# Optimization experiments

Hardware: AMD Instinct MI355X
Metric: run time of the kernel (lower is better)

Reference implementation:

```python
import jax, jax.numpy as jnp
import numpy as np
from jax import lax

C = 256
POOL = 7
NUM_CLASSES = 81
D = NUM_CLASSES - 1
STRIDES = (4, 8, 16, 32)
DEC_MULT = (0.1, 0.1, 0.2, 0.2)  # decode_settings: multipliers on raw deltas
LOG_MAX = float(np.log(1000.0 / 16.0))


def setup_inputs() -> dict:
    key = jax.random.key(0)
    ks = jax.random.split(key, 16)
    n, Rp = 2, 512
    R = n * Rp
    img = 800.0
    cx = jax.random.uniform(ks[0], (R,), minval=0.0, maxval=img)
    cy = jax.random.uniform(ks[1], (R,), minval=0.0, maxval=img)
    w = jax.random.uniform(ks[2], (R,), minval=16.0, maxval=300.0)
    h = jax.random.uniform(ks[3], (R,), minval=16.0, maxval=300.0)
    x1 = jnp.clip(cx - w / 2, 0.0, img - 1.0)
    y1 = jnp.clip(cy - h / 2, 0.0, img - 1.0)
    x2 = jnp.minimum(jnp.maximum(cx + w / 2, x1 + 1.0), img)
    y2 = jnp.minimum(jnp.maximum(cy + h / 2, y1 + 1.0), img)
    proposals = jnp.stack([x1, y1, x2, y2], -1)
    imidx = jnp.repeat(jnp.arange(n, dtype=jnp.int32), Rp)
    fmaps = {}
    for li, s in enumerate(STRIDES):
        hw = int(800 // s)
        fmaps[f"fmap{li}"] = jax.random.normal(ks[4 + li], (n, hw, hw, C), jnp.float32)
    c1, clin = C * POOL * POOL, 1024
    def lin(k, fi, fo):
        return (jax.random.normal(k, (fi, fo), jnp.float32) / np.sqrt(fi).astype(np.float32),
                jnp.zeros((fo,), jnp.float32))
    W0, b0 = lin(ks[8], c1, clin)
    W1, b1 = lin(ks[9], clin, clin)
    Wc, bc = lin(ks[10], clin, NUM_CLASSES)
    Wr, br = lin(ks[11], clin, NUM_CLASSES * 4)
    imsizes = jnp.full((n, 2), img, jnp.float32)  # (h, w) per image
    return dict(proposals=proposals, imidx=imidx, **fmaps,
                W0=W0, b0=b0, W1=W1, b1=b1, Wc=Wc, bc=bc, Wr=Wr, br=br,
                imsizes=imsizes, score_thr=0.05, iou_thr=0.5, imtop=100, min_size=1.0)


def _roi_align_level(fmap, boxes, imidx, stride):
    # fmap [n,H,W,C], boxes [R,4] xyxy in image coords; 1 sample per bin, bilinear.
    n, H, W, c = fmap.shape
    s = 1.0 / stride
    x1, y1, x2, y2 = boxes[:, 0] * s, boxes[:, 1] * s, boxes[:, 2] * s, boxes[:, 3] * s
    g = (jnp.arange(POOL, dtype=jnp.float32) + 0.5) / POOL  # bin centers in [0,1]
    xs = x1[:, None] + g[None, :] * (x2 - x1)[:, None] - 0.5  # [R,POOL]
    ys = y1[:, None] + g[None, :] * (y2 - y1)[:, None] - 0.5
    R = boxes.shape[0]
    xx = jnp.broadcast_to(xs[:, None, :], (R, POOL, POOL))
    yy = jnp.broadcast_to(ys[:, :, None], (R, POOL, POOL))
    x0f, y0f = jnp.floor(xx), jnp.floor(yy)
    wx, wy = xx - x0f, yy - y0f
    x0 = jnp.clip(x0f.astype(jnp.int32), 0, W - 1)
    x1i = jnp.clip(x0f.astype(jnp.int32) + 1, 0, W - 1)
    y0 = jnp.clip(y0f.astype(jnp.int32), 0, H - 1)
    y1i = jnp.clip(y0f.astype(jnp.int32) + 1, 0, H - 1)
    ii = imidx[:, None, None]
    v00 = fmap[ii, y0, x0]; v01 = fmap[ii, y0, x1i]
    v10 = fmap[ii, y1i, x0]; v11 = fmap[ii, y1i, x1i]  # each [R,POOL,POOL,C]
    wx, wy = wx[..., None], wy[..., None]
    return (v00 * (1 - wx) * (1 - wy) + v01 * wx * (1 - wy)
            + v10 * (1 - wx) * wy + v11 * wx * wy)


def _forward(proposals, imidx, fmaps, W0, b0, W1, b1, Wc, bc, Wr, br,
             imsizes, score_thr, iou_thr, imtop, min_size):
    R = proposals.shape[0]
    pw = proposals[:, 2] - proposals[:, 0]
    ph = proposals[:, 3] - proposals[:, 1]
    # FPN level assignment (torchvision canonical formula)
    lvl = jnp.floor(4.0 + jnp.log2(jnp.sqrt(pw * ph) / 224.0 + 1e-6))
    lvl = jnp.clip(lvl, 2, 5).astype(jnp.int32) - 2
    pooled = jnp.zeros((R, POOL, POOL, C), fmaps[0].dtype)
    for k, (fm, st) in enumerate(zip(fmaps, STRIDES)):
        pk = _roi_align_level(fm, proposals, imidx, st)
        pooled = jnp.where((lvl == k)[:, None, None, None], pk, pooled)
    # two-FC head + cls/reg
    x = pooled.reshape(R, -1)
    x = jax.nn.relu(x @ W0 + b0)
    x = jax.nn.relu(x @ W1 + b1)
    reg = (x @ Wr + br).reshape(R, NUM_CLASSES, 4)[:, 1:]      # [R,D,4]
    scr = jax.nn.softmax(x @ Wc + bc, axis=-1)[:, 1:]          # [R,D]
    cls = jnp.broadcast_to(jnp.arange(1, NUM_CLASSES, dtype=jnp.int32), (R, D))
    # decode boxes (proposal cwh + weighted deltas, log-space clamp)
    cx = (proposals[:, 0] + proposals[:, 2]) * 0.5
    cy = (proposals[:, 1] + proposals[:, 3]) * 0.5
    dx = reg[..., 0] * DEC_MULT[0]
    dy = reg[..., 1] * DEC_MULT[1]
    dw = jnp.minimum(reg[..., 2] * DEC_MULT[2], LOG_MAX)
    dh = jnp.minimum(reg[..., 3] * DEC_MULT[3], LOG_MAX)
    ncx = dx * pw[:, None] + cx[:, None]
    ncy = dy * ph[:, None] + cy[:, None]
    nw = jnp.exp(dw) * pw[:, None]
    nh = jnp.exp(dh) * ph[:, None]
    hb = imsizes[imidx, 0][:, None]
    wb = imsizes[imidx, 1][:, None]
    bx1 = jnp.clip(ncx - nw / 2, 0.0, wb); bx2 = jnp.clip(ncx + nw / 2, 0.0, wb)
    by1 = jnp.clip(ncy - nh / 2, 0.0, hb); by2 = jnp.clip(ncy + nh / 2, 0.0, hb)
    boxes = jnp.stack([bx1, by1, bx2, by2], -1)                # [R,D,4]
    valid = (scr > score_thr) & (bx2 - bx1 >= min_size) & (by2 - by1 >= min_size)
    # flatten roi-class pairs; class-offset boxes = torchvision batched_nms trick
    M = R * D
    boxes_f = boxes.reshape(M, 4)
    scr_f = scr.reshape(M)
    cls_f = cls.reshape(M)
    valid_f = valid.reshape(M)
    imidx_f = jnp.repeat(imidx, D)
    off = cls_f.astype(boxes_f.dtype)[:, None] * (jnp.max(imsizes) + 2.0)
    bo = boxes_f + off
    areas = (bo[:, 2] - bo[:, 0]) * (bo[:, 3] - bo[:, 1])
    def nms(scores0):
        def step(scores, _):
            i = jnp.argmax(scores)
            s = scores[i]
            b = bo[i]
            iw = jnp.clip(jnp.minimum(b[2], bo[:, 2]) - jnp.maximum(b[0], bo[:, 0]), 0.0)
            ih = jnp.clip(jnp.minimum(b[3], bo[:, 3]) - jnp.maximum(b[1], bo[:, 1]), 0.0)
            inter = iw * ih
            iou = inter / (areas[i] + areas - inter + 1e-6)
            scores = jnp.where(iou > iou_thr, -1.0, scores)
            scores = scores.at[i].set(-1.0)
            return scores, (i, s)
        _, (idx, s) = lax.scan(step, scores0, None, length=imtop)
        return idx, s
    n = imsizes.shape[0]
    ob, osc, ocl = [], [], []
    for i in range(n):
        s0 = jnp.where(valid_f & (imidx_f == i), scr_f, -1.0)
        idx, s = nms(s0)
        keep = s > 0.0  # padded slots have score <= 0
        ob.append(jnp.where(keep[:, None], boxes_f[idx], 0.0))
        osc.append(jnp.where(keep, s, 0.0))
        ocl.append(jnp.where(keep, cls_f[idx], -1))
    return jnp.stack(ob), jnp.stack(osc), jnp.stack(ocl)


def reference(proposals, imidx, fmap0, fmap1, fmap2, fmap3, W0, b0, W1, b1,
              Wc, bc, Wr, br, imsizes, score_thr, iou_thr, imtop, min_size):
    return _forward(proposals, imidx, (fmap0, fmap1, fmap2, fmap3), W0, b0, W1,
                    b1, Wc, bc, Wr, br, imsizes, score_thr, iou_thr, int(imtop),
                    min_size)
```

## Files before the change

kernel.cpp:

```cpp
#include <hip/hip_runtime.h>
#include <math.h>

#define CCH 256
#define NPOOL 7
#define NCLS 81
#define DCLS 80
#define NHEAD 512
#define FLOG_MAX 4.1351666f

typedef _Float16 half8 __attribute__((ext_vector_type(8)));
typedef _Float16 half4 __attribute__((ext_vector_type(4)));
typedef float floatx4 __attribute__((ext_vector_type(4)));

__global__ void zero_k(float4* __restrict__ p, int count4)
{
    int i = blockIdx.x * blockDim.x + threadIdx.x;
    if (i < count4) p[i] = make_float4(0.f, 0.f, 0.f, 0.f);
}

__device__ __forceinline__ void roi_setup(
    const float* __restrict__ prop, const int* __restrict__ imidx,
    const float* __restrict__ f0, const float* __restrict__ f1,
    const float* __restrict__ f2, const float* __restrict__ f3,
    int h0, int h1, int h2, int h3, int b,
    const float*& base, int& W, size_t& o00, size_t& o01, size_t& o10, size_t& o11,
    float& w00, float& w01, float& w10, float& w11)
{
    int roi = b / 49, p = b % 49;
    int py = p / 7, px = p % 7;

    const float* pr = prop + (size_t)roi * 4;
    float x1 = pr[0], y1 = pr[1], x2 = pr[2], y2 = pr[3];
    float pw = x2 - x1, ph = y2 - y1;

    float lv = floorf(4.0f + log2f(sqrtf(pw * ph) / 224.0f + 1e-6f));
    lv = fminf(fmaxf(lv, 2.0f), 5.0f);
    int lvl = (int)lv - 2;

    const float* fm; int H; float s;
    if (lvl == 0)      { fm = f0; H = h0; s = 0.25f;    }
    else if (lvl == 1) { fm = f1; H = h1; s = 0.125f;   }
    else if (lvl == 2) { fm = f2; H = h2; s = 0.0625f;  }
    else               { fm = f3; H = h3; s = 0.03125f; }
    W = H;

    float xs1 = x1 * s, ys1 = y1 * s, xs2 = x2 * s, ys2 = y2 * s;
    float gx = (px + 0.5f) / 7.0f, gy = (py + 0.5f) / 7.0f;
    float xx = xs1 + gx * (xs2 - xs1) - 0.5f;
    float yy = ys1 + gy * (ys2 - ys1) - 0.5f;
    float x0f = floorf(xx), y0f = floorf(yy);
    float wx = xx - x0f, wy = yy - y0f;
    int x0i = min(max((int)x0f, 0), W - 1);
    int x1i = min(max((int)x0f + 1, 0), W - 1);
    int y0i = min(max((int)y0f, 0), H - 1);
    int y1i = min(max((int)y0f + 1, 0), H - 1);

    int ii = imidx[roi];
    base = fm + (size_t)ii * H * W * CCH;
    o00 = ((size_t)y0i * W + x0i) * CCH;
    o01 = ((size_t)y0i * W + x1i) * CCH;
    o10 = ((size_t)y1i * W + x0i) * CCH;
    o11 = ((size_t)y1i * W + x1i) * CCH;
    w00 = (1.0f - wx) * (1.0f - wy);
    w01 = wx * (1.0f - wy);
    w10 = (1.0f - wx) * wy;
    w11 = wx * wy;
}

__global__ void roi_align_k(const float* __restrict__ prop,
                            const int* __restrict__ imidx,
                            const float* __restrict__ f0,
                            const float* __restrict__ f1,
                            const float* __restrict__ f2,
                            const float* __restrict__ f3,
                            int h0, int h1, int h2, int h3,
                            float* __restrict__ pooled)
{
    int b = blockIdx.x, c = threadIdx.x;
    const float* base; int W; size_t o00, o01, o10, o11;
    float w00, w01, w10, w11;
    roi_setup(prop, imidx, f0, f1, f2, f3, h0, h1, h2, h3, b,
              base, W, o00, o01, o10, o11, w00, w01, w10, w11);
    float v = base[o00 + c] * w00 + base[o01 + c] * w01
            + base[o10 + c] * w10 + base[o11 + c] * w11;
    pooled[(size_t)b * CCH + c] = v;
}

__device__ __forceinline__ void roi_f16v4_body(
    const float* __restrict__ prop, const int* __restrict__ imidx,
    const float* __restrict__ f0, const float* __restrict__ f1,
    const float* __restrict__ f2, const float* __restrict__ f3,
    int h0, int h1, int h2, int h3, int bb, int t,
    _Float16* __restrict__ poolH, _Float16* __restrict__ poolL)
{
    int b = bb * 4 + (t >> 6);
    int lane = t & 63;
    const float* base; int W; size_t o00, o01, o10, o11;
    float w00, w01, w10, w11;
    roi_setup(prop, imidx, f0, f1, f2, f3, h0, h1, h2, h3, b,
              base, W, o00, o01, o10, o11, w00, w01, w10, w11);

    int c4 = lane * 4;
    float4 v00 = *(const float4*)(base + o00 + c4);
    float4 v01 = *(const float4*)(base + o01 + c4);
    float4 v10 = *(const float4*)(base + o10 + c4);
    float4 v11 = *(const float4*)(base + o11 + c4);
    const float* p00 = (const float*)&v00;
    const float* p01 = (const float*)&v01;
    const float* p10 = (const float*)&v10;
    const float* p11 = (const float*)&v11;

    half4 h, l;
#pragma unroll
    for (int e = 0; e < 4; ++e) {
        float v = p00[e] * w00 + p01[e] * w01 + p10[e] * w10 + p11[e] * w11;
        _Float16 hh = (_Float16)v;
        h[e] = hh;
        l[e] = (_Float16)(v - (float)hh);
    }
    size_t idx = (size_t)b * CCH + c4;
    *(half4*)(poolH + idx) = h;
    *(half4*)(poolL + idx) = l;
}

__device__ __forceinline__ void conv_fast_body(
    const float* __restrict__ W, _Float16* __restrict__ WtH,
    _Float16* __restrict__ WtL, int K, int N, int k0, int n0, int t,
    float (*sh)[65])
{
#pragma unroll
    for (int p = 0; p < 4; ++p) {
        int idx = p * 256 + t;
        int kr = idx >> 4, nc = (idx & 15) * 4;
        float4 v = *(const float4*)(W + (size_t)(k0 + kr) * N + n0 + nc);
        sh[kr][nc + 0] = v.x; sh[kr][nc + 1] = v.y;
        sh[kr][nc + 2] = v.z; sh[kr][nc + 3] = v.w;
    }
    __syncthreads();
#pragma unroll
    for (int p = 0; p < 4; ++p) {
        int idx = p * 256 + t;
        int nr = idx >> 4, kc = (idx & 15) * 4;
        half4 h, l;
#pragma unroll
        for (int i = 0; i < 4; ++i) {
            float v = sh[kc + i][nr];
            _Float16 hh = (_Float16)v;
            h[i] = hh;
            l[i] = (_Float16)(v - (float)hh);
        }
        *(half4*)(WtH + (size_t)(n0 + nr) * K + k0 + kc) = h;
        *(half4*)(WtL + (size_t)(n0 + nr) * K + k0 + kc) = l;
    }
}

__device__ __forceinline__ void conv_guard_body(
    const float* __restrict__ W, _Float16* __restrict__ WtH,
    _Float16* __restrict__ WtL, int K, int N, int Kt, int rowofs,
    int k0, int n0, int t, float (*sh)[65])
{
#pragma unroll
    for (int p = 0; p < 4; ++p) {
        int idx = p * 256 + t;
        int kr = idx >> 4, nc = (idx & 15) * 4;
#pragma unroll
        for (int e = 0; e < 4; ++e) {
            int nn = n0 + nc + e;
            sh[kr][nc + e] = (nn < N) ? W[(size_t)(k0 + kr) * N + nn] : 0.0f;
        }
    }
    __syncthreads();
#pragma unroll
    for (int p = 0; p < 4; ++p) {
        int idx = p * 256 + t;
        int nr = idx >> 4, kc = (idx & 15) * 4;
        if (n0 + nr < N) {
            half4 h, l;
#pragma unroll
            for (int i = 0; i < 4; ++i) {
                float v = sh[kc + i][nr];
                _Float16 hh = (_Float16)v;
                h[i] = hh;
                l[i] = (_Float16)(v - (float)hh);
            }
            *(half4*)(WtH + (size_t)(rowofs + n0 + nr) * Kt + k0 + kc) = h;
            *(half4*)(WtL + (size_t)(rowofs + n0 + nr) * Kt + k0 + kc) = l;
        }
    }
}

__global__ __launch_bounds__(256) void pre_uber_k(
    const float* __restrict__ prop, const int* __restrict__ imidx,
    const float* __restrict__ f0, const float* __restrict__ f1,
    const float* __restrict__ f2, const float* __restrict__ f3,
    int h0, int h1, int h2, int h3,
    _Float16* __restrict__ poolH, _Float16* __restrict__ poolL,
    const float* __restrict__ W0, _Float16* __restrict__ W0tH, _Float16* __restrict__ W0tL,
    const float* __restrict__ W1, _Float16* __restrict__ W1tH, _Float16* __restrict__ W1tL,
    const float* __restrict__ Wc, const float* __restrict__ Wr,
    _Float16* __restrict__ WheadtH, _Float16* __restrict__ WheadtL,
    float4* __restrict__ zp, int zc4,
    int* __restrict__ cntp, int ncnt,
    int R, int K0, int CL)
{
    __shared__ float sh[64][65];
    int b = blockIdx.x, t = threadIdx.x;

    if (blockIdx.x == 0 && t < ncnt) cntp[t] = 0;

    int NB_ROI = (R * 49) / 4;
    int KT0 = K0 / 64, NT0 = CL / 64;
    int NB_CW0 = KT0 * NT0;
    int KT1 = CL / 64;
    int NB_CW1 = KT1 * KT1;
    int NTc = (NCLS + 63) / 64;
    int NB_CWc = KT1 * NTc;
    int NTr = (NCLS * 4 + 63) / 64;
    int NB_CWr = KT1 * NTr;

    if (b < NB_ROI) {
        roi_f16v4_body(prop, imidx, f0, f1, f2, f3, h0, h1, h2, h3, b, t,
                       poolH, poolL);
        return;
    }
    b -= NB_ROI;
    if (b < NB_CW0) {
        int k0 = (b % KT0) * 64, n0 = (b / KT0) * 64;
        conv_fast_body(W0, W0tH, W0tL, K0, CL, k0, n0, t, sh);
        return;
    }
    b -= NB_CW0;
    if (b < NB_CW1) {
        int k0 = (b % KT1) * 64, n0 = (b / KT1) * 64;
        conv_fast_body(W1, W1tH, W1tL, CL, CL, k0, n0, t, sh);
        return;
    }
    b -= NB_CW1;
    if (b < NB_CWc) {
        int k0 = (b % KT1) * 64, n0 = (b / KT1) * 64;
        conv_guard_body(Wc, WheadtH, WheadtL, CL, NCLS, CL, 0, k0, n0, t, sh);
        return;
    }
    b -= NB_CWc;
    if (b < NB_CWr) {
        int k0 = (b % KT1) * 64, n0 = (b / KT1) * 64;
        conv_guard_body(Wr, WheadtH, WheadtL, CL, NCLS * 4, CL, NCLS, k0, n0, t, sh);
        return;
    }
    b -= NB_CWr;
    {
        int i = b * 256 + t;
        if (i < zc4) zp[i] = make_float4(0.f, 0.f, 0.f, 0.f);
    }
}

__global__ void act_split_k(const float* __restrict__ acc,
                            const float* __restrict__ bias,
                            _Float16* __restrict__ outH,
                            _Float16* __restrict__ outL,
                            int total, int CL)
{
    int i = (blockIdx.x * blockDim.x + threadIdx.x) * 4;
    if (i >= total) return;
    int b = i % CL;
    float4 v = *(const float4*)(acc + i);
    float4 bb = *(const float4*)(bias + b);
    const float* pv = (const float*)&v;
    const float* pb = (const float*)&bb;
    half4 h, l;
#pragma unroll
    for (int e = 0; e < 4; ++e) {
        float f = fmaxf(pv[e] + pb[e], 0.0f);
        _Float16 hh = (_Float16)f;
        h[e] = hh;
        l[e] = (_Float16)(f - (float)hh);
    }
    *(half4*)(outH + i) = h;
    *(half4*)(outL + i) = l;
}

__device__ __forceinline__ void dma16(const _Float16* g, _Float16* l)
{
    __builtin_amdgcn_global_load_lds(
        (const __attribute__((address_space(1))) unsigned int*)g,
        (__attribute__((address_space(3))) unsigned int*)l, 16, 0, 0);
}

#define LDKE 32
#define DKQ_SWZ(lane)  ((((lane) & 3) ^ (((lane) >> 3) & 3)) << 3)
#define FK_SWZ(lane)   (((((lane) >> 4) ^ (((lane) >> 1) & 3))) << 3)

__global__ __launch_bounds__(256) void gemm_mfma_split_k(
    const _Float16* __restrict__ Ah, const _Float16* __restrict__ Al,
    const _Float16* __restrict__ Bh, const _Float16* __restrict__ Bl,
    float* __restrict__ Cacc, int M, int N, int K, int Kc, int SP)
{
    __shared__ _Float16 sAh[128 * LDKE], sAl[128 * LDKE];
    __shared__ _Float16 sBh[64 * LDKE],  sBl[64 * LDKE];

    int bid = blockIdx.x;
    int z = bid % SP;
    int q = bid / SP;
    int NT = N >> 6;
    int nn = q % NT;
    int m = q / NT;
    int m0 = m * 128, n0 = nn * 64;
    int kb = z * Kc;
    int ke = min(K, kb + Kc);

    int t = threadIdx.x;
    int lane = t & 63, w = t >> 6;
    int wr = w >> 1, wc = w & 1;
    int fr = lane & 15;
    int fk = FK_SWZ(lane);

    int drowA = w * 32 + (lane >> 2);
    int drowB = w * 16 + (lane >> 2);
    int dkq = DKQ_SWZ(lane);
    const _Float16* gAh = Ah + (size_t)(m0 + drowA) * K + dkq;
    const _Float16* gAl = Al + (size_t)(m0 + drowA) * K + dkq;
    const _Float16* gBh = Bh + (size_t)(n0 + drowB) * K + dkq;
    const _Float16* gBl = Bl + (size_t)(n0 + drowB) * K + dkq;
    size_t rowskip = (size_t)16 * K;

    _Float16* lAh0 = &sAh[(w * 2 + 0) * 512];
    _Float16* lAh1 = &sAh[(w * 2 + 1) * 512];
    _Float16* lAl0 = &sAl[(w * 2 + 0) * 512];
    _Float16* lAl1 = &sAl[(w * 2 + 1) * 512];
    _Float16* lBh  = &sBh[w * 512];
    _Float16* lBl  = &sBl[w * 512];

    floatx4 acc[4][2] = {};

    for (int k0 = kb; k0 < ke; k0 += 32) {
        dma16(gAh + k0, lAh0);
        dma16(gAh + rowskip + k0, lAh1);
        dma16(gAl + k0, lAl0);
        dma16(gAl + rowskip + k0, lAl1);
        dma16(gBh + k0, lBh);
        dma16(gBl + k0, lBl);
        __syncthreads();

        half8 ah[4], al[4], bh[2], bl[2];
#pragma unroll
        for (int i = 0; i < 4; ++i) {
            int ar = wr * 64 + i * 16 + fr;
            ah[i] = *(const half8*)&sAh[ar * LDKE + fk];
            al[i] = *(const half8*)&sAl[ar * LDKE + fk];
        }
#pragma unroll
        for (int j = 0; j < 2; ++j) {
            int bcc = wc * 32 + j * 16 + fr;
            bh[j] = *(const half8*)&sBh[bcc * LDKE + fk];
            bl[j] = *(const half8*)&sBl[bcc * LDKE + fk];
        }
#pragma unroll
        for (int i = 0; i < 4; ++i)
#pragma unroll
            for (int j = 0; j < 2; ++j) {
                acc[i][j] = __builtin_amdgcn_mfma_f32_16x16x32_f16(ah[i], bh[j], acc[i][j], 0, 0, 0);
                acc[i][j] = __builtin_amdgcn_mfma_f32_16x16x32_f16(ah[i], bl[j], acc[i][j], 0, 0, 0);
                acc[i][j] = __builtin_amdgcn_mfma_f32_16x16x32_f16(al[i], bh[j], acc[i][j], 0, 0, 0);
            }
        __syncthreads();
    }

    int rbase = (lane >> 4) * 4;
#pragma unroll
    for (int i = 0; i < 4; ++i)
#pragma unroll
        for (int j = 0; j < 2; ++j) {
            int col = n0 + wc * 32 + j * 16 + fr;
#pragma unroll
            for (int r = 0; r < 4; ++r) {
                int row = m0 + wr * 64 + i * 16 + rbase + r;
                atomicAdd(&Cacc[(size_t)row * N + col], acc[i][j][r]);
            }
        }
}

__global__ __launch_bounds__(256) void gemm_mfma_fused64_k(
    const _Float16* __restrict__ Ah, const _Float16* __restrict__ Al,
    const _Float16* __restrict__ Bh, const _Float16* __restrict__ Bl,
    const float* __restrict__ bias,
    float* __restrict__ Cout,
    _Float16* __restrict__ outH, _Float16* __restrict__ outL,
    int M, int N, int K, int mode)
{
    __shared__ _Float16 sAh[2][64 * LDKE], sAl[2][64 * LDKE];
    __shared__ _Float16 sBh[2][64 * LDKE], sBl[2][64 * LDKE];

    int m0 = blockIdx.y * 64, n0 = blockIdx.x * 64;
    int t = threadIdx.x;
    int lane = t & 63, w = t >> 6;
    int wr = w >> 1, wc = w & 1;
    int fr = lane & 15;
    int fk = FK_SWZ(lane);

    int drow = w * 16 + (lane >> 2);
    int dkq = DKQ_SWZ(lane);
    const _Float16* gAh = Ah + (size_t)(m0 + drow) * K + dkq;
    const _Float16* gAl = Al + (size_t)(m0 + drow) * K + dkq;
    const _Float16* gBh = Bh + (size_t)(n0 + drow) * K + dkq;
    const _Float16* gBl = Bl + (size_t)(n0 + drow) * K + dkq;
    int lofs = w * 512;

    int nt = K >> 5;

    dma16(gAh + 0, &sAh[0][lofs]);
    dma16(gAl + 0, &sAl[0][lofs]);
    dma16(gBh + 0, &sBh[0][lofs]);
    dma16(gBl + 0, &sBl[0][lofs]);
    __syncthreads();

    floatx4 acc[2][2] = {};

    for (int tt = 0; tt < nt; ++tt) {
        int c = tt & 1, nb = c ^ 1;
        if (tt + 1 < nt) {
            int k1 = (tt + 1) << 5;
            dma16(gAh + k1, &sAh[nb][lofs]);
            dma16(gAl + k1, &sAl[nb][lofs]);
            dma16(gBh + k1, &sBh[nb][lofs]);
            dma16(gBl + k1, &sBl[nb][lofs]);
        }

        half8 ah[2], av[2], bh[2], bv[2];
#pragma unroll
        for (int i = 0; i < 2; ++i) {
            int ar = wr * 32 + i * 16 + fr;
            ah[i] = *(const half8*)&sAh[c][ar * LDKE + fk];
            av[i] = *(const half8*)&sAl[c][ar * LDKE + fk];
            int bc = wc * 32 + i * 16 + fr;
            bh[i] = *(const half8*)&sBh[c][bc * LDKE + fk];
            bv[i] = *(const half8*)&sBl[c][bc * LDKE + fk];
        }
#pragma unroll
        for (int i = 0; i < 2; ++i)
#pragma unroll
            for (int j = 0; j < 2; ++j) {
                acc[i][j] = __builtin_amdgcn_mfma_f32_16x16x32_f16(ah[i], bh[j], acc[i][j], 0, 0, 0);
                acc[i][j] = __builtin_amdgcn_mfma_f32_16x16x32_f16(ah[i], bv[j], acc[i][j], 0, 0, 0);
                acc[i][j] = __builtin_amdgcn_mfma_f32_16x16x32_f16(av[i], bh[j], acc[i][j], 0, 0, 0);
            }
        __syncthreads();
    }

    int rbase = (lane >> 4) * 4;
#pragma unroll
    for (int i = 0; i < 2; ++i)
#pragma unroll
        for (int j = 0; j < 2; ++j) {
            int col = n0 + wc * 32 + j * 16 + fr;
#pragma unroll
            for (int r = 0; r < 4; ++r) {
                int row = m0 + wr * 32 + i * 16 + rbase + r;
                float v = acc[i][j][r];
                if (mode == 0) {
                    Cout[(size_t)row * N + col] = v;
                } else {
                    float f = fmaxf(v + bias[col], 0.0f);
                    _Float16 hh = (_Float16)f;
                    outH[(size_t)row * N + col] = hh;
                    outL[(size_t)row * N + col] = (_Float16)(f - (float)hh);
                }
            }
        }
}

__global__ __launch_bounds__(256) void gemm_splitk_k(const float* __restrict__ A,
                                                     const float* __restrict__ B,
                                                     const float* __restrict__ abias,
                                                     float* __restrict__ Cacc,
                                                     int M, int N, int K, int Kc)
{
    __shared__ float Ast[16][68];
    __shared__ float Bs[16][68];

    int m0 = blockIdx.y * 64, n0 = blockIdx.x * 64;
    int kb = blockIdx.z * Kc;
    int ke = min(K, kb + Kc);
    int tid = threadIdx.x;
    int tx = tid & 15, ty = tid >> 4;
    int arow = tid >> 2, akq = (tid & 3) << 2;
    int bcol = tid & 63, bk = tid >> 6;

    const float* Arow = A + (size_t)(m0 + arow) * K;
    bool nfull = (n0 + 64 <= N);

    float acc[4][4] = {};

    for (int k0 = kb; k0 < ke; k0 += 16) {
        float4 av = *(const float4*)(Arow + k0 + akq);
        if (abias) {
            av.x = fmaxf(av.x + abias[k0 + akq + 0], 0.0f);
            av.y = fmaxf(av.y + abias[k0 + akq + 1], 0.0f);
            av.z = fmaxf(av.z + abias[k0 + akq + 2], 0.0f);
            av.w = fmaxf(av.w + abias[k0 + akq + 3], 0.0f);
        }
        float bv[4];
        if (nfull) {
#pragma unroll
            for (int e = 0; e < 4; ++e)
                bv[e] = B[(size_t)(k0 + bk * 4 + e) * N + n0 + bcol];
        } else {
            bool ok = (n0 + bcol) < N;
#pragma unroll
            for (int e = 0; e < 4; ++e)
                bv[e] = ok ? B[(size_t)(k0 + bk * 4 + e) * N + n0 + bcol] : 0.0f;
        }
        __syncthreads();
        Ast[akq + 0][arow] = av.x;
        Ast[akq + 1][arow] = av.y;
        Ast[akq + 2][arow] = av.z;
        Ast[akq + 3][arow] = av.w;
#pragma unroll
        for (int e = 0; e < 4; ++e) Bs[bk * 4 + e][bcol] = bv[e];
        __syncthreads();

#pragma unroll
        for (int kk = 0; kk < 16; ++kk) {
            float4 af = *(const float4*)&Ast[kk][ty * 4];
            float4 bf = *(const float4*)&Bs[kk][tx * 4];
            float a_[4] = {af.x, af.y, af.z, af.w};
            float b_[4] = {bf.x, bf.y, bf.z, bf.w};
#pragma unroll
            for (int i = 0; i < 4; ++i)
#pragma unroll
                for (int j = 0; j < 4; ++j)
                    acc[i][j] = fmaf(a_[i], b_[j], acc[i][j]);
        }
    }

#pragma unroll
    for (int i = 0; i < 4; ++i) {
        int row = m0 + ty * 4 + i;
#pragma unroll
        for (int j = 0; j < 4; ++j) {
            int col = n0 + tx * 4 + j;
            if (col < N) atomicAdd(&Cacc[(size_t)row * N + col], acc[i][j]);
        }
    }
}

__global__ void softmax_k(const float* __restrict__ logits, int ldl,
                          const float* __restrict__ bc,
                          float* __restrict__ scr)
{
    int r = blockIdx.x;
    int t = threadIdx.x;
    const float* row = logits + (size_t)r * ldl;

    float v0 = row[t] + bc[t];
    float v1 = (t + 64 < NCLS) ? (row[t + 64] + bc[t + 64]) : -INFINITY;
    float m = fmaxf(v0, v1);
#pragma unroll
    for (int o = 32; o > 0; o >>= 1) m = fmaxf(m, __shfl_down(m, o));
    m = __shfl(m, 0);

    float e0 = expf(v0 - m);
    float e1 = (t + 64 < NCLS) ? expf(v1 - m) : 0.0f;
    float sum = e0 + e1;
#pragma unroll
    for (int o = 32; o > 0; o >>= 1) sum += __shfl_down(sum, o);
    sum = __shfl(sum, 0);
    float inv = 1.0f / sum;

    if (t >= 1)        scr[(size_t)r * DCLS + (t - 1)]  = e0 * inv;
    if (t + 64 < NCLS) scr[(size_t)r * DCLS + (t + 63)] = e1 * inv;
}

__global__ __launch_bounds__(256) void compact_k(
    const float* __restrict__ head, int ldh, int regofs,
    const float* __restrict__ bc,
    const float* __restrict__ br,
    const float* __restrict__ prop,
    const int* __restrict__ imidx,
    const float* __restrict__ imsz,
    const float* __restrict__ score_thr_p,
    const float* __restrict__ min_size_p,
    int* __restrict__ cntp,
    int* __restrict__ cidx,
    float* __restrict__ cscore,
    float* __restrict__ cbo,
    float* __restrict__ cbox,
    float* __restrict__ carea,
    int M, int n, int R)
{
    int wid = threadIdx.x >> 6, t = threadIdx.x & 63;
    int r = blockIdx.x * 4 + wid;
    if (r >= R) return;

    const float* row = head + (size_t)r * ldh;
    float v0 = row[t] + bc[t];
    float v1 = (t + 64 < NCLS) ? (row[t + 64] + bc[t + 64]) : -INFINITY;
    float m = fmaxf(v0, v1);
#pragma unroll
    for (int o = 32; o > 0; o >>= 1) m = fmaxf(m, __shfl_down(m, o));
    m = __shfl(m, 0);

    float e0 = expf(v0 - m);
    float e1 = (t + 64 < NCLS) ? expf(v1 - m) : 0.0f;
    float sum = e0 + e1;
#pragma unroll
    for (int o = 32; o > 0; o >>= 1) sum += __shfl_down(sum, o);
    sum = __shfl(sum, 0);
    float inv = 1.0f / sum;

    float score_thr = score_thr_p[0];
    float min_size  = min_size_p[0];
    float immax = imsz[0];
    for (int q = 1; q < 2 * n; ++q) immax = fmaxf(immax, imsz[q]);

    int img = imidx[r];
    int base = img * M;
    const float* pr = prop + (size_t)r * 4;
    float pw = pr[2] - pr[0], ph = pr[3] - pr[1];
    float cx = (pr[0] + pr[2]) * 0.5f, cy = (pr[1] + pr[3]) * 0.5f;
    float hbound = imsz[img * 2 + 0];
    float wbound = imsz[img * 2 + 1];

#pragma unroll
    for (int pass = 0; pass < 2; ++pass) {
        int cls; float s; bool active;
        if (pass == 0) { cls = t;      s = e0 * inv; active = (t >= 1); }
        else           { cls = t + 64; s = e1 * inv; active = (t + 64 < NCLS); }
        if (!active || s <= score_thr) continue;

        const float* rg_ = head + (size_t)r * ldh + regofs + cls * 4;
        const float* bb = br + cls * 4;
        float dx = (rg_[0] + bb[0]) * 0.1f;
        float dy = (rg_[1] + bb[1]) * 0.1f;
        float dw = fminf((rg_[2] + bb[2]) * 0.2f, FLOG_MAX);
        float dh = fminf((rg_[3] + bb[3]) * 0.2f, FLOG_MAX);
        float ncx = dx * pw + cx;
        float ncy = dy * ph + cy;
        float nw = expf(dw) * pw;
        float nh = expf(dh) * ph;
        float bx1 = fminf(fmaxf(ncx - nw * 0.5f, 0.0f), wbound);
        float bx2 = fminf(fmaxf(ncx + nw * 0.5f, 0.0f), wbound);
        float by1 = fminf(fmaxf(ncy - nh * 0.5f, 0.0f), hbound);
        float by2 = fminf(fmaxf(ncy + nh * 0.5f, 0.0f), hbound);
        if (bx2 - bx1 < min_size || by2 - by1 < min_size) continue;

        float off = (float)cls * (immax + 2.0f);
        int j = r * DCLS + cls - 1;
        int p = atomicAdd(&cntp[img], 1);
        cidx[base + p] = j;
        cscore[base + p] = s;
        cbox[(size_t)(base + p) * 4 + 0] = bx1;
        cbox[(size_t)(base + p) * 4 + 1] = by1;
        cbox[(size_t)(base + p) * 4 + 2] = bx2;
        cbox[(size_t)(base + p) * 4 + 3] = by2;
        cbo[(size_t)(base + p) * 4 + 0] = bx1 + off;
        cbo[(size_t)(base + p) * 4 + 1] = by1 + off;
        cbo[(size_t)(base + p) * 4 + 2] = bx2 + off;
        cbo[(size_t)(base + p) * 4 + 3] = by2 + off;
        carea[base + p] = (bx2 - bx1) * (by2 - by1);
    }
}

#define NMS_T 1024
#define NMS_SORTMAX 4096
#define NMS_AMAX 512
__global__ __launch_bounds__(NMS_T) void nms_pick_k(
    const float* __restrict__ iou_thr_p,
    const int* __restrict__ cntp,
    int* __restrict__ cidx,
    float* __restrict__ cscore,
    float* __restrict__ cbo,
    float* __restrict__ cbox,
    float* __restrict__ carea,
    float* __restrict__ out,
    int M, int n, int imtop)
{
// ... 144 lines not shown
                    if (os > b2 || (os == b2 && og < g2)) { b2 = os; g2 = og; l2 = ol; }
                }
                if (lane == 0) {
                    f_sc = b2;
                    if (b2 > 0.0f) {
                        int lp = l2;
                        size_t oslot = (size_t)img * imtop + it;
                        ob[oslot * 4 + 0] = cbox[(size_t)(base + lp) * 4 + 0];
                        ob[oslot * 4 + 1] = cbox[(size_t)(base + lp) * 4 + 1];
                        ob[oslot * 4 + 2] = cbox[(size_t)(base + lp) * 4 + 2];
                        ob[oslot * 4 + 3] = cbox[(size_t)(base + lp) * 4 + 3];
                        osc[oslot] = b2;
                        ocl[oslot] = (float)(g2 % DCLS + 1);
                        f_o0 = cbo[(size_t)(base + lp) * 4 + 0];
                        f_o1 = cbo[(size_t)(base + lp) * 4 + 1];
                        f_o2 = cbo[(size_t)(base + lp) * 4 + 2];
                        f_o3 = cbo[(size_t)(base + lp) * 4 + 3];
                        f_ar = carea[base + lp];
                        cscore[base + lp] = -1.0f;
                    }
                }
            }
            __syncthreads();
            if (f_sc <= 0.0f) break;

            float b0 = f_o0, b1 = f_o1, b2_ = f_o2, b3 = f_o3, ai = f_ar;
            for (int p = t; p < K; p += T) {
                float c0 = cbo[(size_t)(base + p) * 4 + 0];
                float c1 = cbo[(size_t)(base + p) * 4 + 1];
                float c2 = cbo[(size_t)(base + p) * 4 + 2];
                float c3 = cbo[(size_t)(base + p) * 4 + 3];
                float iw = fmaxf(fminf(b2_, c2) - fmaxf(b0, c0), 0.0f);
                float ih = fmaxf(fminf(b3, c3) - fmaxf(b1, c1), 0.0f);
                float inter = iw * ih;
                float iou = inter / (ai + carea[base + p] - inter + 1e-6f);
                if (iou > iou_thr) cscore[base + p] = -1.0f;
            }
            __syncthreads();
        }
    }

    for (int q = it + t; q < imtop; q += T) {
        size_t oslot = (size_t)img * imtop + q;
        ob[oslot * 4 + 0] = 0.0f;
        ob[oslot * 4 + 1] = 0.0f;
        ob[oslot * 4 + 2] = 0.0f;
        ob[oslot * 4 + 3] = 0.0f;
        osc[oslot] = 0.0f;
        ocl[oslot] = -1.0f;
    }
}

__global__ __launch_bounds__(NMS_T) void nms_k(
    const float* __restrict__ scr,
    const float* __restrict__ prop,
    const int* __restrict__ imidx,
    const float* __restrict__ head, int ldh, int regofs,
    const float* __restrict__ br,
    const float* __restrict__ imsz,
    const float* __restrict__ score_thr_p,
    const float* __restrict__ min_size_p,
    const float* __restrict__ iou_thr_p,
    int* __restrict__ cidx,
    float* __restrict__ cscore,
    float* __restrict__ cbo,
    float* __restrict__ cbox,
    float* __restrict__ carea,
    float* __restrict__ out,
    int M, int n, int imtop)
{
    int img = blockIdx.x;
    int t = threadIdx.x;
    const int T = NMS_T;
    const int NW = NMS_T / 64;
    int lane = t & 63, wid = t >> 6;

    __shared__ int cnt;
    __shared__ float ws_sc[NW];
    __shared__ int ws_g[NW], ws_p[NW];
    __shared__ float f_sc, f_o0, f_o1, f_o2, f_o3, f_ar;

    if (t == 0) cnt = 0;
    __syncthreads();

    float score_thr = score_thr_p[0];
    float min_size  = min_size_p[0];
    float iou_thr   = iou_thr_p[0];
    float immax = imsz[0];
    for (int q = 1; q < 2 * n; ++q) immax = fmaxf(immax, imsz[q]);

    int base = img * M;
    for (int j = t; j < M; j += T) {
        int r = j / DCLS;
        if (imidx[r] != img) continue;
        float s = scr[j];
        if (s <= score_thr) continue;

        int cls = j - r * DCLS + 1;
        const float* pr = prop + (size_t)r * 4;
        float pw = pr[2] - pr[0], ph = pr[3] - pr[1];
        float cx = (pr[0] + pr[2]) * 0.5f, cy = (pr[1] + pr[3]) * 0.5f;
        const float* rg_ = head + (size_t)r * ldh + regofs + cls * 4;
        const float* bb = br + cls * 4;
        float dx = (rg_[0] + bb[0]) * 0.1f;
        float dy = (rg_[1] + bb[1]) * 0.1f;
        float dw = fminf((rg_[2] + bb[2]) * 0.2f, FLOG_MAX);
        float dh = fminf((rg_[3] + bb[3]) * 0.2f, FLOG_MAX);
        float ncx = dx * pw + cx;
        float ncy = dy * ph + cy;
        float nw = expf(dw) * pw;
        float nh = expf(dh) * ph;
        float hbound = imsz[img * 2 + 0];
        float wbound = imsz[img * 2 + 1];
        float bx1 = fminf(fmaxf(ncx - nw * 0.5f, 0.0f), wbound);
        float bx2 = fminf(fmaxf(ncx + nw * 0.5f, 0.0f), wbound);
        float by1 = fminf(fmaxf(ncy - nh * 0.5f, 0.0f), hbound);
        float by2 = fminf(fmaxf(ncy + nh * 0.5f, 0.0f), hbound);
        if (bx2 - bx1 < min_size || by2 - by1 < min_size) continue;

        float off = (float)cls * (immax + 2.0f);
        int p = atomicAdd(&cnt, 1);
        cidx[base + p] = j;
        cscore[base + p] = s;
        cbox[(size_t)(base + p) * 4 + 0] = bx1;
        cbox[(size_t)(base + p) * 4 + 1] = by1;
        cbox[(size_t)(base + p) * 4 + 2] = bx2;
        cbox[(size_t)(base + p) * 4 + 3] = by2;
        cbo[(size_t)(base + p) * 4 + 0] = bx1 + off;
        cbo[(size_t)(base + p) * 4 + 1] = by1 + off;
        cbo[(size_t)(base + p) * 4 + 2] = bx2 + off;
        cbo[(size_t)(base + p) * 4 + 3] = by2 + off;
        carea[base + p] = (bx2 - bx1) * (by2 - by1);
    }
    __syncthreads();
    int K = cnt;

    float* ob  = out;
    float* osc = out + (size_t)n * imtop * 4;
    float* ocl = out + (size_t)n * imtop * 5;

    int it = 0;
    for (; it < imtop; ++it) {
        float best = -1e30f; int bg = 0x7fffffff; int bl = -1;
        for (int p = t; p < K; p += T) {
            float sv = cscore[base + p];
            int g = cidx[base + p];
            if (sv > best || (sv == best && g < bg)) { best = sv; bg = g; bl = p; }
        }
#pragma unroll
        for (int o = 32; o > 0; o >>= 1) {
            float os = __shfl_down(best, o);
            int   og = __shfl_down(bg, o);
            int   ol = __shfl_down(bl, o);
            if (os > best || (os == best && og < bg)) { best = os; bg = og; bl = ol; }
        }
        if (lane == 0) { ws_sc[wid] = best; ws_g[wid] = bg; ws_p[wid] = bl; }
        __syncthreads();
        if (wid == 0) {
            float b2 = (lane < NW) ? ws_sc[lane] : -1e30f;
            int   g2 = (lane < NW) ? ws_g[lane] : 0x7fffffff;
            int   l2 = (lane < NW) ? ws_p[lane] : -1;
#pragma unroll
            for (int o = NW / 2; o > 0; o >>= 1) {
                float os = __shfl_down(b2, o);
                int   og = __shfl_down(g2, o);
                int   ol = __shfl_down(l2, o);
                if (os > b2 || (os == b2 && og < g2)) { b2 = os; g2 = og; l2 = ol; }
            }
            if (lane == 0) {
                f_sc = b2;
                if (b2 > 0.0f) {
                    int lp = l2;
                    size_t oslot = (size_t)img * imtop + it;
                    ob[oslot * 4 + 0] = cbox[(size_t)(base + lp) * 4 + 0];
                    ob[oslot * 4 + 1] = cbox[(size_t)(base + lp) * 4 + 1];
                    ob[oslot * 4 + 2] = cbox[(size_t)(base + lp) * 4 + 2];
                    ob[oslot * 4 + 3] = cbox[(size_t)(base + lp) * 4 + 3];
                    osc[oslot] = b2;
                    ocl[oslot] = (float)(g2 % DCLS + 1);
                    f_o0 = cbo[(size_t)(base + lp) * 4 + 0];
                    f_o1 = cbo[(size_t)(base + lp) * 4 + 1];
                    f_o2 = cbo[(size_t)(base + lp) * 4 + 2];
                    f_o3 = cbo[(size_t)(base + lp) * 4 + 3];
                    f_ar = carea[base + lp];
                    cscore[base + lp] = -1.0f;
                }
            }
        }
        __syncthreads();
        if (f_sc <= 0.0f) break;

        float b0 = f_o0, b1 = f_o1, b2_ = f_o2, b3 = f_o3, ai = f_ar;
        for (int p = t; p < K; p += T) {
            float c0 = cbo[(size_t)(base + p) * 4 + 0];
            float c1 = cbo[(size_t)(base + p) * 4 + 1];
            float c2 = cbo[(size_t)(base + p) * 4 + 2];
            float c3 = cbo[(size_t)(base + p) * 4 + 3];
            float iw = fmaxf(fminf(b2_, c2) - fmaxf(b0, c0), 0.0f);
            float ih = fmaxf(fminf(b3, c3) - fmaxf(b1, c1), 0.0f);
            float inter = iw * ih;
            float iou = inter / (ai + carea[base + p] - inter + 1e-6f);
            if (iou > iou_thr) cscore[base + p] = -1.0f;
        }
        __syncthreads();
    }

    for (int q = it + t; q < imtop; q += T) {
        size_t oslot = (size_t)img * imtop + q;
        ob[oslot * 4 + 0] = 0.0f;
        ob[oslot * 4 + 1] = 0.0f;
        ob[oslot * 4 + 2] = 0.0f;
        ob[oslot * 4 + 3] = 0.0f;
        osc[oslot] = 0.0f;
        ocl[oslot] = -1.0f;
    }
}

extern "C" void kernel_launch(void* const* d_in, const int* in_sizes, int n_in,
                              void* d_out, int out_size, void* d_ws, size_t ws_size,
                              hipStream_t stream)
{
    const float* prop   = (const float*)d_in[0];
    const int*   imidx  = (const int*)d_in[1];
    const float* f0     = (const float*)d_in[2];
    const float* f1     = (const float*)d_in[3];
    const float* f2     = (const float*)d_in[4];
    const float* f3     = (const float*)d_in[5];
    const float* W0     = (const float*)d_in[6];
    const float* b0     = (const float*)d_in[7];
    const float* W1     = (const float*)d_in[8];
    const float* b1     = (const float*)d_in[9];
    const float* Wc     = (const float*)d_in[10];
    const float* bc     = (const float*)d_in[11];
    const float* Wr     = (const float*)d_in[12];
    const float* br     = (const float*)d_in[13];
    const float* imsz   = (const float*)d_in[14];
    const float* sthr   = (const float*)d_in[15];
    const float* ithr   = (const float*)d_in[16];
    const float* msz    = (const float*)d_in[18];

    int R = in_sizes[1];
    int n = in_sizes[14] / 2;
    int imtop = out_size / (n * 6);
    int M = R * DCLS;
    int K0 = NPOOL * NPOOL * CCH;
    int CL = in_sizes[7];

    int h0 = (int)(sqrtf((float)(in_sizes[2] / (n * CCH))) + 0.5f);
    int h1 = (int)(sqrtf((float)(in_sizes[3] / (n * CCH))) + 0.5f);
    int h2 = (int)(sqrtf((float)(in_sizes[4] / (n * CCH))) + 0.5f);
    int h3 = (int)(sqrtf((float)(in_sizes[5] / (n * CCH))) + 0.5f);

    float* outf = (float*)d_out;

    size_t szPool  = (size_t)R * K0 * 2;
    size_t szX     = (size_t)R * CL * 4;
    size_t szHead  = (size_t)R * NHEAD * 4;
    size_t szWh    = (size_t)NHEAD * CL * 2;
    size_t szXh    = (size_t)R * CL * 2;
    size_t szW1t   = (size_t)CL * CL * 2;
    size_t szScr   = (size_t)R * DCLS * 4;

    size_t needed = 4 * szPool + 2 * szX + szHead + 2 * szWh
                  + 4 * szXh + 2 * szW1t + szScr;

    int splitK0 = 8;
    bool mfma_ok = (ws_size >= needed) && (R % 128 == 0) && (CL % 128 == 0)
                 && (K0 % (splitK0 * 32) == 0) && (CL % 32 == 0)
                 && ((R * 49) % 4 == 0) && (K0 % 64 == 0) && (CL % 64 == 0)
                 && (R % 4 == 0);

    if (mfma_ok) {
        uint8_t* w = (uint8_t*)d_ws;
        size_t o = 0;
        _Float16* poolH   = (_Float16*)(w + o); o += szPool;
        _Float16* poolL   = (_Float16*)(w + o); o += szPool;
        _Float16* W0tH    = (_Float16*)(w + o); o += szPool;
        _Float16* W0tL    = (_Float16*)(w + o); o += szPool;
        float*    x0acc   = (float*)(w + o);    o += szX;
        float*    unused  = (float*)(w + o);    o += szX;
        float*    headacc = (float*)(w + o);    o += szHead;
        _Float16* WheadtH = (_Float16*)(w + o); o += szWh;
        _Float16* WheadtL = (_Float16*)(w + o); o += szWh;
        _Float16* x0H     = (_Float16*)(w + o); o += szXh;
        _Float16* x0L     = (_Float16*)(w + o); o += szXh;
        _Float16* x1H     = (_Float16*)(w + o); o += szXh;
        _Float16* x1L     = (_Float16*)(w + o); o += szXh;
        _Float16* W1tH    = (_Float16*)(w + o); o += szW1t;
        _Float16* W1tL    = (_Float16*)(w + o); o += szW1t;
        float*    scr     = (float*)(w + o);
        (void)unused;

        int* cnt = (int*)scr;

        int*   cidx   = (int*)d_ws;
        float* cscore = (float*)(cidx + (size_t)n * M);
        float* cbo    = cscore + (size_t)n * M;
        float* cbox   = cbo + (size_t)n * M * 4;
        float* carea  = cbox + (size_t)n * M * 4;

        {
            int NB_ROI = (R * 49) / 4;
            int NB_CW0 = (K0 / 64) * (CL / 64);
            int NB_CW1 = (CL / 64) * (CL / 64);
            int NB_CWc = (CL / 64) * ((NCLS + 63) / 64);
            int NB_CWr = (CL / 64) * ((NCLS * 4 + 63) / 64);
            int zc4    = (int)(szX / 16);
            int NB_Z   = (zc4 + 255) / 256;
            int NB = NB_ROI + NB_CW0 + NB_CW1 + NB_CWc + NB_CWr + NB_Z;
            pre_uber_k<<<dim3(NB), dim3(256), 0, stream>>>(
                prop, imidx, f0, f1, f2, f3, h0, h1, h2, h3,
                poolH, poolL,
                W0, W0tH, W0tL,
                W1, W1tH, W1tL,
                Wc, Wr, WheadtH, WheadtL,
                (float4*)x0acc, zc4,
                cnt, n,
                R, K0, CL);
        }
        gemm_mfma_split_k<<<dim3(splitK0 * (R / 128) * (CL / 64)), dim3(256), 0, stream>>>(
            poolH, poolL, W0tH, W0tL, x0acc, R, CL, K0, K0 / splitK0, splitK0);
        act_split_k<<<dim3((R * CL / 4 + 255) / 256), dim3(256), 0, stream>>>(
            x0acc, b0, x0H, x0L, R * CL, CL);
        gemm_mfma_fused64_k<<<dim3(CL / 64, R / 64), dim3(256), 0, stream>>>(
            x0H, x0L, W1tH, W1tL, b1, nullptr, x1H, x1L, R, CL, CL, 1);
        gemm_mfma_fused64_k<<<dim3(NHEAD / 64, R / 64), dim3(256), 0, stream>>>(
            x1H, x1L, WheadtH, WheadtL, nullptr, headacc, nullptr, nullptr, R, NHEAD, CL, 0);
        compact_k<<<dim3(R / 4), dim3(256), 0, stream>>>(
            headacc, NHEAD, NCLS, bc, br, prop, imidx, imsz, sthr, msz,
            cnt, cidx, cscore, cbo, cbox, carea, M, n, R);
        nms_pick_k<<<dim3(n), dim3(NMS_T), 0, stream>>>(
            ithr, cnt, cidx, cscore, cbo, cbox, carea, outf, M, n, imtop);
    } else {
        float* ws = (float*)d_ws;
        size_t off = 0;
        float* pooled  = ws + off; off += (size_t)R * K0;
        float* x0acc   = ws + off; off += (size_t)R * CL;
        float* x1acc   = ws + off; off += (size_t)R * CL;
        float* logits  = ws + off; off += (size_t)R * NCLS;
        off = (off + 3) & ~(size_t)3;
        float* reg     = ws + off; off += (size_t)R * NCLS * 4;
        float* scr     = ws + off; off += (size_t)R * DCLS;

        int*   cidx   = (int*)ws;
        float* cscore = (float*)(cidx + (size_t)n * M);
        float* cbo    = cscore + (size_t)n * M;
        float* cbox   = cbo + (size_t)n * M * 4;
        float* carea  = cbox + (size_t)n * M * 4;

        {
            size_t zcount = (size_t)(reg + (size_t)R * NCLS * 4 - x0acc);
            int c4 = (int)(zcount / 4);
            zero_k<<<dim3((c4 + 255) / 256), dim3(256), 0, stream>>>((float4*)x0acc, c4);
        }
        roi_align_k<<<dim3(R * 49), dim3(256), 0, stream>>>(
            prop, imidx, f0, f1, f2, f3, h0, h1, h2, h3, pooled);
        gemm_splitk_k<<<dim3(CL / 64, R / 64, 8), dim3(256), 0, stream>>>(
            pooled, W0, nullptr, x0acc, R, CL, K0, 1568);
        gemm_splitk_k<<<dim3(CL / 64, R / 64, 4), dim3(256), 0, stream>>>(
            x0acc, W1, b0, x1acc, R, CL, CL, 256);
        gemm_splitk_k<<<dim3((NCLS + 63) / 64, R / 64, 8), dim3(256), 0, stream>>>(
            x1acc, Wc, b1, logits, R, NCLS, CL, 128);
        gemm_splitk_k<<<dim3((NCLS * 4 + 63) / 64, R / 64, 4), dim3(256), 0, stream>>>(
            x1acc, Wr, b1, reg, R, NCLS * 4, CL, 256);
        softmax_k<<<dim3(R), dim3(64), 0, stream>>>(logits, NCLS, bc, scr);
        nms_k<<<dim3(n), dim3(NMS_T), 0, stream>>>(
            scr, prop, imidx, reg, NCLS * 4, 0, br, imsz, sthr, msz, ithr,
            cidx, cscore, cbo, cbox, carea, outf, M, n, imtop);
    }
}
```

Measured before the change: 385.2 us.

## Widen FC0 split-K GEMM tile to 128x128 and move W1/head conversion into it

The FC0 split-K GEMM tile grows from 128x64 to 128x128 per block, so each wave computes a 4x4 grid of MFMA fragments. This raises arithmetic intensity and halves the number of atomic-add blocks per K slice. The W1 and head weight conversion blocks move from the pre-processing uber kernel into the GEMM launch as extra trailing blocks, which shortens the first kernel's critical path. In exchange each thread holds more accumulator registers, which may lower occupancy, and fewer GEMM blocks means less parallelism across the device.

Result: no change. 378.1 us (-1.8%).

```diff
diff --git a/kernel.cpp b/kernel.cpp
--- a/kernel.cpp
+++ b/kernel.cpp
@@ -196,9 +196,6 @@
     int h0, int h1, int h2, int h3,
     _Float16* __restrict__ poolH, _Float16* __restrict__ poolL,
     const float* __restrict__ W0, _Float16* __restrict__ W0tH, _Float16* __restrict__ W0tL,
-    const float* __restrict__ W1, _Float16* __restrict__ W1tH, _Float16* __restrict__ W1tL,
-    const float* __restrict__ Wc, const float* __restrict__ Wr,
-    _Float16* __restrict__ WheadtH, _Float16* __restrict__ WheadtL,
     float4* __restrict__ zp, int zc4,
     int* __restrict__ cntp, int ncnt,
     int R, int K0, int CL)
@@ -211,12 +208,6 @@
     int NB_ROI = (R * 49) / 4;
     int KT0 = K0 / 64, NT0 = CL / 64;
     int NB_CW0 = KT0 * NT0;
-    int KT1 = CL / 64;
-    int NB_CW1 = KT1 * KT1;
-    int NTc = (NCLS + 63) / 64;
-    int NB_CWc = KT1 * NTc;
-    int NTr = (NCLS * 4 + 63) / 64;
-    int NB_CWr = KT1 * NTr;
 
     if (b < NB_ROI) {
         roi_f16v4_body(prop, imidx, f0, f1, f2, f3, h0, h1, h2, h3, b, t,
@@ -230,24 +221,6 @@
         return;
     }
     b -= NB_CW0;
-    if (b < NB_CW1) {
-        int k0 = (b % KT1) * 64, n0 = (b / KT1) * 64;
-        conv_fast_body(W1, W1tH, W1tL, CL, CL, k0, n0, t, sh);
-        return;
-    }
-    b -= NB_CW1;
-    if (b < NB_CWc) {
-        int k0 = (b % KT1) * 64, n0 = (b / KT1) * 64;
-        conv_guard_body(Wc, WheadtH, WheadtL, CL, NCLS, CL, 0, k0, n0, t, sh);
-        return;
-    }
-    b -= NB_CWc;
-    if (b < NB_CWr) {
-        int k0 = (b % KT1) * 64, n0 = (b / KT1) * 64;
-        conv_guard_body(Wr, WheadtH, WheadtL, CL, NCLS * 4, CL, NCLS, k0, n0, t, sh);
-        return;
-    }
-    b -= NB_CWr;
     {
         int i = b * 256 + t;
         if (i < zc4) zp[i] = make_float4(0.f, 0.f, 0.f, 0.f);
@@ -290,74 +263,107 @@
 #define DKQ_SWZ(lane)  ((((lane) & 3) ^ (((lane) >> 3) & 3)) << 3)
 #define FK_SWZ(lane)   (((((lane) >> 4) ^ (((lane) >> 1) & 3))) << 3)
 
-__global__ __launch_bounds__(256) void gemm_mfma_split_k(
+__global__ __launch_bounds__(256) void gemm_fc0_conv_k(
     const _Float16* __restrict__ Ah, const _Float16* __restrict__ Al,
     const _Float16* __restrict__ Bh, const _Float16* __restrict__ Bl,
-    float* __restrict__ Cacc, int M, int N, int K, int Kc, int SP)
-{
-    __shared__ _Float16 sAh[128 * LDKE], sAl[128 * LDKE];
-    __shared__ _Float16 sBh[64 * LDKE],  sBl[64 * LDKE];
+    float* __restrict__ Cacc, int M, int N, int K, int Kc, int SP, int nbg,
+    const float* __restrict__ W1, _Float16* __restrict__ W1tH, _Float16* __restrict__ W1tL,
+    const float* __restrict__ Wc, const float* __restrict__ Wr,
+    _Float16* __restrict__ WheadtH, _Float16* __restrict__ WheadtL, int CL)
+{
+    __shared__ __align__(16) char smem[4 * 128 * LDKE * 2];
+
+    int t = threadIdx.x;
+
+    if (blockIdx.x >= nbg) {
+        float (*sh)[65] = (float(*)[65])smem;
+        int b = blockIdx.x - nbg;
+        int KT1 = CL / 64;
+        int NB_CW1 = KT1 * KT1;
+        int NB_CWc = KT1 * ((NCLS + 63) / 64);
+        if (b < NB_CW1) {
+            int k0 = (b % KT1) * 64, n0 = (b / KT1) * 64;
+            conv_fast_body(W1, W1tH, W1tL, CL, CL, k0, n0, t, sh);
+            return;
+        }
+        b -= NB_CW1;
+        if (b < NB_CWc) {
+            int k0 = (b % KT1) * 64, n0 = (b / KT1) * 64;
+            conv_guard_body(Wc, WheadtH, WheadtL, CL, NCLS, CL, 0, k0, n0, t, sh);
+            return;
+        }
+        b -= NB_CWc;
+        {
+            int k0 = (b % KT1) * 64, n0 = (b / KT1) * 64;
+            conv_guard_body(Wr, WheadtH, WheadtL, CL, NCLS * 4, CL, NCLS, k0, n0, t, sh);
+            return;
+        }
+    }
+
+    _Float16* sAh = (_Float16*)smem;
+    _Float16* sAl = sAh + 128 * LDKE;
+    _Float16* sBh = sAl + 128 * LDKE;
+    _Float16* sBl = sBh + 128 * LDKE;
 
     int bid = blockIdx.x;
     int z = bid % SP;
     int q = bid / SP;
-    int NT = N >> 6;
+    int NT = N >> 7;
     int nn = q % NT;
     int m = q / NT;
-    int m0 = m * 128, n0 = nn * 64;
+    int m0 = m * 128, n0 = nn * 128;
     int kb = z * Kc;
     int ke = min(K, kb + Kc);
 
-    int t = threadIdx.x;
     int lane = t & 63, w = t >> 6;
     int wr = w >> 1, wc = w & 1;
     int fr = lane & 15;
     int fk = FK_SWZ(lane);
 
-    int drowA = w * 32 + (lane >> 2);
-    int drowB = w * 16 + (lane >> 2);
+    int drow = w * 32 + (lane >> 2);
     int dkq = DKQ_SWZ(lane);
-    const _Float16* gAh = Ah + (size_t)(m0 + drowA) * K + dkq;
-    const _Float16* gAl = Al + (size_t)(m0 + drowA) * K + dkq;
-    const _Float16* gBh = Bh + (size_t)(n0 + drowB) * K + dkq;
-    const _Float16* gBl = Bl + (size_t)(n0 + drowB) * K + dkq;
+    const _Float16* gAh = Ah + (size_t)(m0 + drow) * K + dkq;
+    const _Float16* gAl = Al + (size_t)(m0 + drow) * K + dkq;
+    const _Float16* gBh = Bh + (size_t)(n0 + drow) * K + dkq;
+    const _Float16* gBl = Bl + (size_t)(n0 + drow) * K + dkq;
     size_t rowskip = (size_t)16 * K;
 
     _Float16* lAh0 = &sAh[(w * 2 + 0) * 512];
     _Float16* lAh1 = &sAh[(w * 2 + 1) * 512];
     _Float16* lAl0 = &sAl[(w * 2 + 0) * 512];
     _Float16* lAl1 = &sAl[(w * 2 + 1) * 512];
-    _Float16* lBh  = &sBh[w * 512];
-    _Float16* lBl  = &sBl[w * 512];
-
-    floatx4 acc[4][2] = {};
+    _Float16* lBh0 = &sBh[(w * 2 + 0) * 512];
+    _Float16* lBh1 = &sBh[(w * 2 + 1) * 512];
+    _Float16* lBl0 = &sBl[(w * 2 + 0) * 512];
+    _Float16* lBl1 = &sBl[(w * 2 + 1) * 512];
+
+    floatx4 acc[4][4] = {};
 
     for (int k0 = kb; k0 < ke; k0 += 32) {
         dma16(gAh + k0, lAh0);
         dma16(gAh + rowskip + k0, lAh1);
         dma16(gAl + k0, lAl0);
         dma16(gAl + rowskip + k0, lAl1);
-        dma16(gBh + k0, lBh);
-        dma16(gBl + k0, lBl);
+        dma16(gBh + k0, lBh0);
+        dma16(gBh + rowskip + k0, lBh1);
+        dma16(gBl + k0, lBl0);
+        dma16(gBl + rowskip + k0, lBl1);
         __syncthreads();
 
-        half8 ah[4], al[4], bh[2], bl[2];
+        half8 ah[4], al[4], bh[4], bl[4];
 #pragma unroll
         for (int i = 0; i < 4; ++i) {
             int ar = wr * 64 + i * 16 + fr;
             ah[i] = *(const half8*)&sAh[ar * LDKE + fk];
             al[i] = *(const half8*)&sAl[ar * LDKE + fk];
-        }
-#pragma unroll
-        for (int j = 0; j < 2; ++j) {
-            int bcc = wc * 32 + j * 16 + fr;
-            bh[j] = *(const half8*)&sBh[bcc * LDKE + fk];
-            bl[j] = *(const half8*)&sBl[bcc * LDKE + fk];
+            int bc = wc * 64 + i * 16 + fr;
+            bh[i] = *(const half8*)&sBh[bc * LDKE + fk];
+            bl[i] = *(const half8*)&sBl[bc * LDKE + fk];
         }
 #pragma unroll
         for (int i = 0; i < 4; ++i)
 #pragma unroll
-            for (int j = 0; j < 2; ++j) {
+            for (int j = 0; j < 4; ++j) {
                 acc[i][j] = __builtin_amdgcn_mfma_f32_16x16x32_f16(ah[i], bh[j], acc[i][j], 0, 0, 0);
                 acc[i][j] = __builtin_amdgcn_mfma_f32_16x16x32_f16(ah[i], bl[j], acc[i][j], 0, 0, 0);
                 acc[i][j] = __builtin_amdgcn_mfma_f32_16x16x32_f16(al[i], bh[j], acc[i][j], 0, 0, 0);
@@ -369,8 +375,8 @@
 #pragma unroll
     for (int i = 0; i < 4; ++i)
 #pragma unroll
-        for (int j = 0; j < 2; ++j) {
-            int col = n0 + wc * 32 + j * 16 + fr;
+        for (int j = 0; j < 4; ++j) {
+            int col = n0 + wc * 64 + j * 16 + fr;
 #pragma unroll
             for (int r = 0; r < 4; ++r) {
                 int row = m0 + wr * 64 + i * 16 + rbase + r;
@@ -1121,24 +1127,27 @@
         {
             int NB_ROI = (R * 49) / 4;
             int NB_CW0 = (K0 / 64) * (CL / 64);
-            int NB_CW1 = (CL / 64) * (CL / 64);
-            int NB_CWc = (CL / 64) * ((NCLS + 63) / 64);
-            int NB_CWr = (CL / 64) * ((NCLS * 4 + 63) / 64);
             int zc4    = (int)(szX / 16);
             int NB_Z   = (zc4 + 255) / 256;
-            int NB = NB_ROI + NB_CW0 + NB_CW1 + NB_CWc + NB_CWr + NB_Z;
+            int NB = NB_ROI + NB_CW0 + NB_Z;
             pre_uber_k<<<dim3(NB), dim3(256), 0, stream>>>(
                 prop, imidx, f0, f1, f2, f3, h0, h1, h2, h3,
                 poolH, poolL,
                 W0, W0tH, W0tL,
-                W1, W1tH, W1tL,
-                Wc, Wr, WheadtH, WheadtL,
                 (float4*)x0acc, zc4,
                 cnt, n,
                 R, K0, CL);
         }
-        gemm_mfma_split_k<<<dim3(splitK0 * (R / 128) * (CL / 64)), dim3(256), 0, stream>>>(
-            poolH, poolL, W0tH, W0tL, x0acc, R, CL, K0, K0 / splitK0, splitK0);
+        {
+            int nbg = splitK0 * (R / 128) * (CL / 128);
+            int KT1 = CL / 64;
+            int NB_CW1 = KT1 * KT1;
+            int NB_CWc = KT1 * ((NCLS + 63) / 64);
+            int NB_CWr = KT1 * ((NCLS * 4 + 63) / 64);
+            gemm_fc0_conv_k<<<dim3(nbg + NB_CW1 + NB_CWc + NB_CWr), dim3(256), 0, stream>>>(
+                poolH, poolL, W0tH, W0tL, x0acc, R, CL, K0, K0 / splitK0, splitK0, nbg,
+                W1, W1tH, W1tL, Wc, Wr, WheadtH, WheadtL, CL);
+        }
         act_split_k<<<dim3((R * CL / 4 + 255) / 256), dim3(256), 0, stream>>>(
             x0acc, b0, x0H, x0L, R * CL, CL);
         gemm_mfma_fused64_k<<<dim3(CL / 64, R / 64), dim3(256), 0, stream>>>(
```
